# Performance work log

Hardware: AMD Instinct MI355X
Metric: run time of the kernel (lower is better)

The kernel has to match this reference:

```python
import jax, jax.numpy as jnp
import numpy as np

EPS = 1e-8  # StyleGAN instance-norm epsilon
LRELU_SLOPE = 0.2


def setup_inputs() -> dict:
    key = jax.random.key(0)
    ks = jax.random.split(key, 8)
    B, H, W, C, NF, ZD = 8, 64, 64, 512, 512, 512
    x = jax.random.normal(ks[0], (B, H, W, C), dtype=jnp.float32)
    dlatents = jax.random.normal(ks[1], (B, ZD), dtype=jnp.float32)
    noise_map = jax.random.normal(ks[2], (B, H, W, 1), dtype=jnp.float32)
    conv_w = jax.random.normal(ks[3], (C, NF), dtype=jnp.float32) * (1.0 / np.sqrt(C))
    noise_weight = jax.random.normal(ks[4], (1, 1, 1, NF), dtype=jnp.float32) * 0.1
    bias = jax.random.normal(ks[5], (1, 1, 1, NF), dtype=jnp.float32) * 0.1
    dense_w = jax.random.normal(ks[6], (ZD, 2 * NF), dtype=jnp.float32) * (1.0 / np.sqrt(ZD))
    dense_b = jax.random.normal(ks[7], (2 * NF,), dtype=jnp.float32) * 0.1
    return {"x": x, "dlatents": dlatents, "noise_map": noise_map, "conv_w": conv_w,
            "noise_weight": noise_weight, "bias": bias, "dense_w": dense_w, "dense_b": dense_b}


def reference(x, dlatents, noise_map, conv_w, noise_weight, bias, dense_w, dense_b):
    # 1x1 conv, no bias: per-pixel GEMM over channels. [B,H,W,C] @ [C,NF]
    y = jnp.einsum('bhwc,cf->bhwf', x, conv_w)
    # spatial noise (per-channel weight) + bias + leaky relu, fused elementwise
    y = jax.nn.leaky_relu(y + noise_weight * noise_map + bias, LRELU_SLOPE)
    # param-free instance norm over spatial dims (per sample, per channel)
    mu = jnp.mean(y, axis=(1, 2), keepdims=True)
    var = jnp.mean(jnp.square(y - mu), axis=(1, 2), keepdims=True)
    yn = (y - mu) * jax.lax.rsqrt(var + EPS)
    # style modulation: dense(dlatents) -> [B, 2, 1, 1, NF] -> gamma, beta
    gb = dlatents @ dense_w + dense_b
    nf = y.shape[-1]
    gb = gb.reshape(-1, 2, 1, 1, nf)
    gamma, beta = gb[:, 0], gb[:, 1]
    return yn * (1.0 + gamma) + beta
```

## Files before the change

### kernel.cpp

```cpp
#include <hip/hip_runtime.h>

typedef unsigned short u16;
typedef unsigned int u32;
typedef __attribute__((ext_vector_type(8))) short short8;
typedef __attribute__((ext_vector_type(4))) float f32x4;

#define LRELU_SLOPE 0.2f
#define EPS 1e-8f

static __device__ inline u32 cvt_pk_bf16(float lo, float hi) {
    u32 r;
    asm volatile("v_cvt_pk_bf16_f32 %0, %1, %2" : "=v"(r) : "v"(lo), "v"(hi));
    return r;
}
static __device__ inline u16 f2bf(float x) {
    u32 u = __float_as_uint(x);
    u += 0x7FFF + ((u >> 16) & 1);
    return (u16)(u >> 16);
}

__global__ __launch_bounds__(256) void k_twt(const float* __restrict__ w, u16* __restrict__ wt) {
    int t = blockIdx.x * 256 + threadIdx.x;
    int n = t >> 9, k = t & 511;
    wt[n * 512 + k] = f2bf(w[k * 512 + n]);
}

__global__ __launch_bounds__(256) void k_gemm(
    const float* __restrict__ x, const u16* __restrict__ wt,
    const float* __restrict__ noise, const float* __restrict__ nw,
    const float* __restrict__ bias, float* __restrict__ y,
    float* __restrict__ sum, float* __restrict__ sumsq)
{
    __shared__ __align__(16) u16 Al[128 * 64];
    __shared__ __align__(16) u16 Bl[128 * 64];
    const int tid  = threadIdx.x;
    const int lane = tid & 63;
    const int wid  = tid >> 6;
    const int wm   = wid >> 1, wn = wid & 1;
    const int m0   = blockIdx.x * 128;
    const int n0   = blockIdx.y * 128;

    f32x4 acc[4][4] = {};

    for (int kb = 0; kb < 512; kb += 64) {
        #pragma unroll
        for (int j = 0; j < 4; ++j) {
            int uid = j * 256 + tid;
            int row = uid >> 3;
            int cp  = uid & 7;
            int c   = cp ^ (row & 7);
            const float* src = x + (size_t)(m0 + row) * 512 + kb + c * 8;
            float4 v0 = *(const float4*)src;
            float4 v1 = *(const float4*)(src + 4);
            uint4 o;
            o.x = cvt_pk_bf16(v0.x, v0.y);
            o.y = cvt_pk_bf16(v0.z, v0.w);
            o.z = cvt_pk_bf16(v1.x, v1.y);
            o.w = cvt_pk_bf16(v1.z, v1.w);
            *(uint4*)((char*)Al + row * 128 + cp * 16) = o;
        }
        #pragma unroll
        for (int j = 0; j < 4; ++j) {
            int uid = j * 256 + tid;
            int row = uid >> 3;
            int cp  = uid & 7;
            int c   = cp ^ (row & 7);
            uint4 v = *(const uint4*)(wt + (size_t)(n0 + row) * 512 + kb + c * 8);
            *(uint4*)((char*)Bl + row * 128 + cp * 16) = v;
        }
        __syncthreads();
        #pragma unroll
        for (int ks = 0; ks < 2; ++ks) {
            short8 af[4], bf[4];
            const int cidx = ks * 4 + (lane >> 4);
            #pragma unroll
            for (int mi = 0; mi < 4; ++mi) {
                int row = wm * 64 + mi * 16 + (lane & 15);
                af[mi] = *(const short8*)((char*)Al + row * 128 + ((cidx ^ (row & 7)) * 16));
            }
            #pragma unroll
            for (int ni = 0; ni < 4; ++ni) {
                int row = wn * 64 + ni * 16 + (lane & 15);
                bf[ni] = *(const short8*)((char*)Bl + row * 128 + ((cidx ^ (row & 7)) * 16));
            }
            #pragma unroll
            for (int mi = 0; mi < 4; ++mi)
                #pragma unroll
                for (int ni = 0; ni < 4; ++ni)
                    acc[mi][ni] = __builtin_amdgcn_mfma_f32_16x16x32_bf16(
                        af[mi], bf[ni], acc[mi][ni], 0, 0, 0);
        }
        __syncthreads();
    }

    const int b = m0 >> 12;
    float nwv[4], bv[4];
    int colb[4];
    #pragma unroll
    for (int ni = 0; ni < 4; ++ni) {
        int col = n0 + wn * 64 + ni * 16 + (lane & 15);
        colb[ni] = col;
        nwv[ni] = nw[col];
        bv[ni]  = bias[col];
    }
    float ls[4] = {0, 0, 0, 0}, lq[4] = {0, 0, 0, 0};
    #pragma unroll
    for (int mi = 0; mi < 4; ++mi) {
        int rbase = m0 + wm * 64 + mi * 16 + (lane >> 4) * 4;
        #pragma unroll
        for (int r = 0; r < 4; ++r) {
            int row = rbase + r;
            float nz = noise[row];
            #pragma unroll
            for (int ni = 0; ni < 4; ++ni) {
                float v = acc[mi][ni][r] + nwv[ni] * nz + bv[ni];
                v = v > 0.0f ? v : LRELU_SLOPE * v;
                y[(size_t)row * 512 + colb[ni]] = v;
                ls[ni] += v;
                lq[ni] += v * v;
            }
        }
    }
    #pragma unroll
    for (int ni = 0; ni < 4; ++ni) {
        float s = ls[ni], q = lq[ni];
        s += __shfl_xor(s, 16); s += __shfl_xor(s, 32);
        q += __shfl_xor(q, 16); q += __shfl_xor(q, 32);
        if ((lane >> 4) == 0) {
            atomicAdd(&sum[b * 512 + colb[ni]], s);
            atomicAdd(&sumsq[b * 512 + colb[ni]], q);
        }
    }
}

__global__ __launch_bounds__(256) void k_dense(
    const float* __restrict__ dl, const float* __restrict__ dw,
    const float* __restrict__ db, const float* __restrict__ sum,
    const float* __restrict__ sumsq, float* __restrict__ As, float* __restrict__ Cs)
{
    __shared__ float sg[256], sb[256];
    int tid = threadIdx.x;
    int p   = tid >> 3;
    int kc  = tid & 7;
    int t   = blockIdx.x * 32 + p;
    int b   = t >> 9, f = t & 511;
    const float* dlb = dl + b * 512;
    float g = 0.0f, be = 0.0f;
    #pragma unroll 8
    for (int i = 0; i < 64; ++i) {
        int k = kc * 64 + i;
        float dv = dlb[k];
        g  += dv * dw[k * 1024 + f];
        be += dv * dw[k * 1024 + 512 + f];
    }
    sg[tid] = g; sb[tid] = be;
    __syncthreads();
    if (kc == 0) {
        #pragma unroll
        for (int j = 1; j < 8; ++j) { g += sg[tid + j]; be += sb[tid + j]; }
        g  += db[f];
        be += db[512 + f];
        float mu  = sum[t]   * (1.0f / 4096.0f);
        float var = sumsq[t] * (1.0f / 4096.0f) - mu * mu;
        float inv = rsqrtf(var + EPS);
        float A = inv * (1.0f + g);
        As[t] = A;
        Cs[t] = be - mu * A;
    }
}

__global__ __launch_bounds__(256) void k_norm(
    float* __restrict__ y, const float* __restrict__ As, const float* __restrict__ Cs)
{
    size_t i8 = (size_t)(blockIdx.x * 256 + threadIdx.x) * 8;
    int row = (int)(i8 >> 9);
    int f0  = (int)(i8 & 511);
    int b   = row >> 12;
    const float4 a0 = *(const float4*)(As + b * 512 + f0);
    const float4 a1 = *(const float4*)(As + b * 512 + f0 + 4);
    const float4 c0 = *(const float4*)(Cs + b * 512 + f0);
    const float4 c1 = *(const float4*)(Cs + b * 512 + f0 + 4);
    float4 v0 = *(float4*)(y + i8);
    float4 v1 = *(float4*)(y + i8 + 4);
    v0.x = v0.x * a0.x + c0.x;  v0.y = v0.y * a0.y + c0.y;
    v0.z = v0.z * a0.z + c0.z;  v0.w = v0.w * a0.w + c0.w;
    v1.x = v1.x * a1.x + c1.x;  v1.y = v1.y * a1.y + c1.y;
    v1.z = v1.z * a1.z + c1.z;  v1.w = v1.w * a1.w + c1.w;
    *(float4*)(y + i8)     = v0;
    *(float4*)(y + i8 + 4) = v1;
}

extern "C" void kernel_launch(void* const* d_in, const int* in_sizes, int n_in,
                              void* d_out, int out_size, void* d_ws, size_t ws_size,
                              hipStream_t stream) {
    const float* x     = (const float*)d_in[0];
    const float* dl    = (const float*)d_in[1];
    const float* noise = (const float*)d_in[2];
    const float* w     = (const float*)d_in[3];
    const float* nw    = (const float*)d_in[4];
    const float* bias  = (const float*)d_in[5];
    const float* dw    = (const float*)d_in[6];
    const float* db    = (const float*)d_in[7];
    float* out = (float*)d_out;

    char* ws = (char*)d_ws;
    u16*   wt    = (u16*)ws;
    float* sum   = (float*)(ws + 524288);
    float* sumsq = (float*)(ws + 524288 + 16384);
    float* As    = (float*)(ws + 524288 + 32768);
    float* Cs    = (float*)(ws + 524288 + 49152);

    hipMemsetAsync(sum, 0, 32768, stream);
    k_twt  <<<1024, 256, 0, stream>>>(w, wt);
    k_gemm <<<dim3(256, 4), 256, 0, stream>>>(x, wt, noise, nw, bias, out, sum, sumsq);
    k_dense<<<128, 256, 0, stream>>>(dl, dw, db, sum, sumsq, As, Cs);
    k_norm <<<8192, 256, 0, stream>>>(out, As, Cs);
}
```

Before: 202.2 us.

## Double-buffer GEMM tiles with direct-to-LDS weight loads and workgroup swizzle

The GEMM main loop now double-buffers the A and B tiles in LDS. The next x tile is prefetched into registers and the pre-swizzled bf16 weights are streamed straight into LDS with global_load_lds, all while the MFMAs run on the current buffer. This drops one barrier per k-step and hides global load latency. The weight transpose kernel now writes weights already in the XOR-swizzled layout so the direct LDS copy lands correctly. The grid is flattened with a block-index swizzle that groups the four N tiles of an M row for L2 reuse, and the dense style kernel is rewritten as one thread per output with no shared-memory reduction, which gives it far fewer threads.

```diff
diff --git a/kernel.cpp b/kernel.cpp
--- a/kernel.cpp
+++ b/kernel.cpp
@@ -4,6 +4,8 @@
 typedef unsigned int u32;
 typedef __attribute__((ext_vector_type(8))) short short8;
 typedef __attribute__((ext_vector_type(4))) float f32x4;
+typedef const __attribute__((address_space(1))) void gvoid;
+typedef __attribute__((address_space(3))) void lvoid;
 
 #define LRELU_SLOPE 0.2f
 #define EPS 1e-8f
@@ -19,69 +21,86 @@
     return (u16)(u >> 16);
 }
 
-__global__ __launch_bounds__(256) void k_twt(const float* __restrict__ w, u16* __restrict__ wt) {
+__global__ __launch_bounds__(256) void k_twt(const float* __restrict__ w, u16* __restrict__ wts) {
     int t = blockIdx.x * 256 + threadIdx.x;
     int n = t >> 9, k = t & 511;
-    wt[n * 512 + k] = f2bf(w[k * 512 + n]);
-}
-
-__global__ __launch_bounds__(256) void k_gemm(
-    const float* __restrict__ x, const u16* __restrict__ wt,
+    int pos = (k & 448) + ((((k >> 3) ^ n) & 7) << 3) + (k & 7);
+    wts[(size_t)n * 512 + pos] = f2bf(w[(size_t)k * 512 + n]);
+}
+
+__global__ __launch_bounds__(256, 2) void k_gemm(
+    const float* __restrict__ x, const u16* __restrict__ wts,
     const float* __restrict__ noise, const float* __restrict__ nw,
     const float* __restrict__ bias, float* __restrict__ y,
     float* __restrict__ sum, float* __restrict__ sumsq)
 {
-    __shared__ __align__(16) u16 Al[128 * 64];
-    __shared__ __align__(16) u16 Bl[128 * 64];
+    __shared__ __align__(16) u16 Al[2][128 * 64];
+    __shared__ __align__(16) u16 Bl[2][128 * 64];
     const int tid  = threadIdx.x;
     const int lane = tid & 63;
     const int wid  = tid >> 6;
     const int wm   = wid >> 1, wn = wid & 1;
-    const int m0   = blockIdx.x * 128;
-    const int n0   = blockIdx.y * 128;
+    const int wg   = blockIdx.x;
+    const int swz  = (wg & 7) * 128 + (wg >> 3);
+    const int m0   = (swz >> 2) * 128;
+    const int n0   = (swz & 3) * 128;
+
+    const int arow = tid >> 3;
+    const int acp  = tid & 7;
+    const int ac   = acp ^ (arow & 7);
+    const float* asrc = x + (size_t)(m0 + arow) * 512 + ac * 8;
+    const size_t brow0 = (size_t)(n0 + wid * 32 + (lane >> 3)) * 512 + (lane & 7) * 8;
 
     f32x4 acc[4][4] = {};
-
-    for (int kb = 0; kb < 512; kb += 64) {
-        #pragma unroll
-        for (int j = 0; j < 4; ++j) {
-            int uid = j * 256 + tid;
-            int row = uid >> 3;
-            int cp  = uid & 7;
-            int c   = cp ^ (row & 7);
-            const float* src = x + (size_t)(m0 + row) * 512 + kb + c * 8;
-            float4 v0 = *(const float4*)src;
-            float4 v1 = *(const float4*)(src + 4);
-            uint4 o;
-            o.x = cvt_pk_bf16(v0.x, v0.y);
-            o.y = cvt_pk_bf16(v0.z, v0.w);
-            o.z = cvt_pk_bf16(v1.x, v1.y);
-            o.w = cvt_pk_bf16(v1.z, v1.w);
-            *(uint4*)((char*)Al + row * 128 + cp * 16) = o;
-        }
-        #pragma unroll
-        for (int j = 0; j < 4; ++j) {
-            int uid = j * 256 + tid;
-            int row = uid >> 3;
-            int cp  = uid & 7;
-            int c   = cp ^ (row & 7);
-            uint4 v = *(const uint4*)(wt + (size_t)(n0 + row) * 512 + kb + c * 8);
-            *(uint4*)((char*)Bl + row * 128 + cp * 16) = v;
-        }
-        __syncthreads();
+    float4 pa[8];
+
+    #pragma unroll
+    for (int j = 0; j < 4; ++j) {
+        pa[2 * j]     = *(const float4*)(asrc + (size_t)j * 32 * 512);
+        pa[2 * j + 1] = *(const float4*)(asrc + (size_t)j * 32 * 512 + 4);
+    }
+    #pragma unroll
+    for (int i = 0; i < 4; ++i)
+        __builtin_amdgcn_global_load_lds((gvoid*)(wts + brow0 + (size_t)i * 8 * 512),
+                                         (lvoid*)((char*)Bl[0] + wid * 4096 + i * 1024), 16, 0, 0);
+    #pragma unroll
+    for (int j = 0; j < 4; ++j) {
+        uint4 o;
+        o.x = cvt_pk_bf16(pa[2 * j].x, pa[2 * j].y);
+        o.y = cvt_pk_bf16(pa[2 * j].z, pa[2 * j].w);
+        o.z = cvt_pk_bf16(pa[2 * j + 1].x, pa[2 * j + 1].y);
+        o.w = cvt_pk_bf16(pa[2 * j + 1].z, pa[2 * j + 1].w);
+        *(uint4*)((char*)Al[0] + (arow + j * 32) * 128 + acp * 16) = o;
+    }
+    __syncthreads();
+
+    for (int t = 0; t < 8; ++t) {
+        const int cb = t & 1, nb = cb ^ 1;
+        const int kb = (t + 1) * 64;
+        if (t < 7) {
+            #pragma unroll
+            for (int j = 0; j < 4; ++j) {
+                pa[2 * j]     = *(const float4*)(asrc + (size_t)j * 32 * 512 + kb);
+                pa[2 * j + 1] = *(const float4*)(asrc + (size_t)j * 32 * 512 + kb + 4);
+            }
+            #pragma unroll
+            for (int i = 0; i < 4; ++i)
+                __builtin_amdgcn_global_load_lds((gvoid*)(wts + brow0 + (size_t)i * 8 * 512 + kb),
+                                                 (lvoid*)((char*)Bl[nb] + wid * 4096 + i * 1024), 16, 0, 0);
+        }
         #pragma unroll
         for (int ks = 0; ks < 2; ++ks) {
             short8 af[4], bf[4];
             const int cidx = ks * 4 + (lane >> 4);
             #pragma unroll
             for (int mi = 0; mi < 4; ++mi) {
-                int row = wm * 64 + mi * 16 + (lane & 15);
-                af[mi] = *(const short8*)((char*)Al + row * 128 + ((cidx ^ (row & 7)) * 16));
+                int r = wm * 64 + mi * 16 + (lane & 15);
+                af[mi] = *(const short8*)((char*)Al[cb] + r * 128 + ((cidx ^ (r & 7)) * 16));
             }
             #pragma unroll
             for (int ni = 0; ni < 4; ++ni) {
-                int row = wn * 64 + ni * 16 + (lane & 15);
-                bf[ni] = *(const short8*)((char*)Bl + row * 128 + ((cidx ^ (row & 7)) * 16));
+                int r = wn * 64 + ni * 16 + (lane & 15);
+                bf[ni] = *(const short8*)((char*)Bl[cb] + r * 128 + ((cidx ^ (r & 7)) * 16));
             }
             #pragma unroll
             for (int mi = 0; mi < 4; ++mi)
@@ -90,7 +109,18 @@
                     acc[mi][ni] = __builtin_amdgcn_mfma_f32_16x16x32_bf16(
                         af[mi], bf[ni], acc[mi][ni], 0, 0, 0);
         }
-        __syncthreads();
+        if (t < 7) {
+            #pragma unroll
+            for (int j = 0; j < 4; ++j) {
+                uint4 o;
+                o.x = cvt_pk_bf16(pa[2 * j].x, pa[2 * j].y);
+                o.y = cvt_pk_bf16(pa[2 * j].z, pa[2 * j].w);
+                o.z = cvt_pk_bf16(pa[2 * j + 1].x, pa[2 * j + 1].y);
+                o.w = cvt_pk_bf16(pa[2 * j + 1].z, pa[2 * j + 1].w);
+                *(uint4*)((char*)Al[nb] + (arow + j * 32) * 128 + acp * 16) = o;
+            }
+            __syncthreads();
+        }
     }
 
     const int b = m0 >> 12;
@@ -133,40 +163,28 @@
     }
 }
 
-__global__ __launch_bounds__(256) void k_dense(
+__global__ __launch_bounds__(256) void k_gb(
     const float* __restrict__ dl, const float* __restrict__ dw,
     const float* __restrict__ db, const float* __restrict__ sum,
     const float* __restrict__ sumsq, float* __restrict__ As, float* __restrict__ Cs)
 {
-    __shared__ float sg[256], sb[256];
-    int tid = threadIdx.x;
-    int p   = tid >> 3;
-    int kc  = tid & 7;
-    int t   = blockIdx.x * 32 + p;
-    int b   = t >> 9, f = t & 511;
-    const float* dlb = dl + b * 512;
-    float g = 0.0f, be = 0.0f;
-    #pragma unroll 8
-    for (int i = 0; i < 64; ++i) {
-        int k = kc * 64 + i;
+    int f = blockIdx.x * 256 + threadIdx.x;
+    int b = blockIdx.y;
+    const float* dlb = dl + (size_t)b * 512;
+    float g  = db[f];
+    float be = db[512 + f];
+    #pragma unroll 4
+    for (int k = 0; k < 512; ++k) {
         float dv = dlb[k];
-        g  += dv * dw[k * 1024 + f];
-        be += dv * dw[k * 1024 + 512 + f];
-    }
-    sg[tid] = g; sb[tid] = be;
-    __syncthreads();
-    if (kc == 0) {
-        #pragma unroll
-        for (int j = 1; j < 8; ++j) { g += sg[tid + j]; be += sb[tid + j]; }
-        g  += db[f];
-        be += db[512 + f];
-        float mu  = sum[t]   * (1.0f / 4096.0f);
-        float var = sumsq[t] * (1.0f / 4096.0f) - mu * mu;
-        float inv = rsqrtf(var + EPS);
-        float A = inv * (1.0f + g);
-        As[t] = A;
-        Cs[t] = be - mu * A;
-    }
+        g  = fmaf(dv, dw[(size_t)k * 1024 + f], g);
+        be = fmaf(dv, dw[(size_t)k * 1024 + 512 + f], be);
+    }
+    int t = b * 512 + f;
+    float mu  = sum[t]   * (1.0f / 4096.0f);
+    float var = sumsq[t] * (1.0f / 4096.0f) - mu * mu;
+    float A = rsqrtf(var + EPS) * (1.0f + g);
+    As[t] = A;
+    Cs[t] = be - mu * A;
 }
 
 __global__ __launch_bounds__(256) void k_norm(
@@ -204,15 +222,15 @@
     float* out = (float*)d_out;
 
     char* ws = (char*)d_ws;
-    u16*   wt    = (u16*)ws;
+    u16*   wts   = (u16*)ws;
     float* sum   = (float*)(ws + 524288);
-    float* sumsq = (float*)(ws + 524288 + 16384);
-    float* As    = (float*)(ws + 524288 + 32768);
-    float* Cs    = (float*)(ws + 524288 + 49152);
+    float* sumsq = (float*)(ws + 540672);
+    float* As    = (float*)(ws + 557056);
+    float* Cs    = (float*)(ws + 573440);
 
     hipMemsetAsync(sum, 0, 32768, stream);
-    k_twt  <<<1024, 256, 0, stream>>>(w, wt);
-    k_gemm <<<dim3(256, 4), 256, 0, stream>>>(x, wt, noise, nw, bias, out, sum, sumsq);
-    k_dense<<<128, 256, 0, stream>>>(dl, dw, db, sum, sumsq, As, Cs);
-    k_norm <<<8192, 256, 0, stream>>>(out, As, Cs);
-}
+    k_twt <<<1024, 256, 0, stream>>>(w, wts);
+    k_gemm<<<1024, 256, 0, stream>>>(x, wts, noise, nw, bias, out, sum, sumsq);
+    k_gb  <<<dim3(2, 8), 256, 0, stream>>>(dl, dw, db, sum, sumsq, As, Cs);
+    k_norm<<<8192, 256, 0, stream>>>(out, As, Cs);
+}
```

Measured after the change: 247.8 us. 22.5% more time.
